# Optimization experiments

Measured on AMD Instinct MI355X. Metric: run time of the kernel, lower is better.

Reference implementation:

```python
import jax, jax.numpy as jnp
import numpy as np

EMBED_DIM = 512
NUM_HEADS = 8
B, L_Q, L_K = 2, 2048, 2048


def setup_inputs() -> dict:
    key = jax.random.key(0)
    ks = jax.random.split(key, 8)
    s = 0.02  # weight init scale
    return {
        "query": jax.random.normal(ks[0], (B, L_Q, EMBED_DIM), jnp.float32),
        "key":   jax.random.normal(ks[1], (B, L_K, EMBED_DIM), jnp.float32),
        "value": jax.random.normal(ks[2], (B, L_K, EMBED_DIM), jnp.float32),
        "wq": jax.random.normal(ks[3], (EMBED_DIM, EMBED_DIM), jnp.float32) * s,
        "wk": jax.random.normal(ks[4], (EMBED_DIM, EMBED_DIM), jnp.float32) * s,
        "wv": jax.random.normal(ks[5], (EMBED_DIM, EMBED_DIM), jnp.float32) * s,
        "bq": jnp.zeros((EMBED_DIM,), jnp.float32),
        "bk": jnp.zeros((EMBED_DIM,), jnp.float32),
        "bv": jnp.zeros((EMBED_DIM,), jnp.float32),
        "wo": jax.random.normal(ks[6], (EMBED_DIM, EMBED_DIM), jnp.float32) * s,
        "bo": jnp.zeros((EMBED_DIM,), jnp.float32),
    }


def _prob_sparse_mask(query, key, num_heads):
    # Faithful to _prob_QK: max-mean sparsity score, top-k query selection,
    # gather of reduced queries, reduced QK matmul (vectorized, no python loops).
    Bq, Lq, D = query.shape
    Lk = key.shape[1]
    dh = D // num_heads
    n_top = int(np.log(Lk))  # int(np.ceil/np.log) as in source forward: int(np.log(L_K))
    Q = query.reshape(Bq, Lq, num_heads, dh)
    K = key.reshape(Bq, Lk, num_heads, dh)
    Qh = jnp.transpose(Q, (0, 2, 1, 3))                      # [B,H,Lq,dh]
    # NOTE: source does K.transpose(1,2).reshape(B,H,D,L_K) -- a reshape, not a
    # transpose of the last two dims. We replicate that exactly.
    Kr = jnp.transpose(K, (0, 2, 1, 3)).reshape(Bq, num_heads, dh, Lk)  # [B,H,dh,Lk]
    QK = jnp.einsum('bhqd,bhdk->bhqk', Qh, Kr)               # [B,H,Lq,Lk]
    M = QK.max(-1) - QK.sum(-1) / Lk                         # max-mean score [B,H,Lq]
    _, M_top = jax.lax.top_k(M, n_top)                       # [B,H,n_top]
    Q_red = jnp.take_along_axis(Qh, M_top[..., None], axis=2)  # [B,H,n_top,dh]
    QK_red = jnp.einsum('bhtd,bhdk->bhtk', Q_red, Kr)        # [B,H,n_top,Lk]
    # Scatter reduced rows back into a full additive attn mask (zeros elsewhere).
    mask = jnp.zeros((Bq, num_heads, Lq, Lk), QK.dtype)
    bi = jnp.arange(Bq)[:, None, None]
    hi = jnp.arange(num_heads)[None, :, None]
    return mask.at[bi, hi, M_top].set(QK_red)


def reference(query, key, value, wq, wk, wv, bq, bk, bv, wo, bo):
    Bq, Lq, D = query.shape
    Lk = key.shape[1]
    H = NUM_HEADS
    dh = D // H
    mask = _prob_sparse_mask(query, key, H)                  # [B,H,Lq,Lk]
    q = (query @ wq.T + bq).reshape(Bq, Lq, H, dh).transpose(0, 2, 1, 3)
    k = (key @ wk.T + bk).reshape(Bq, Lk, H, dh).transpose(0, 2, 1, 3)
    v = (value @ wv.T + bv).reshape(Bq, Lk, H, dh).transpose(0, 2, 1, 3)
    scores = jnp.einsum('bhqd,bhkd->bhqk', q, k) * (dh ** -0.5) + mask
    attn = jax.nn.softmax(scores, axis=-1)                   # dropout inactive (eval)
    out = jnp.einsum('bhqk,bhkd->bhqd', attn, v)
    out = out.transpose(0, 2, 1, 3).reshape(Bq, Lq, D)
    return out @ wo.T + bo
```

## Files before the change

### kernel.cpp

```cpp
#include <hip/hip_runtime.h>
#include <type_traits>

#define DEV static __device__ __forceinline__

typedef short s16;
typedef __attribute__((ext_vector_type(4))) short short4_t;
typedef __attribute__((ext_vector_type(8))) short short8;
typedef __attribute__((ext_vector_type(4))) float f32x4;

#define NB 2
#define NH 8
#define SL 2048
#define DM 512
#define DH 64
#define NTOP 7
#define LOG2E 1.4426950408889634f
#define NROWS (NB*NH*SL)
#define FSPLIT 2
#define SSPLIT 2

DEV short f2bf(float x){
  union { float f; unsigned u; } v; v.f = x;
  unsigned r = v.u + 0x7fffu + ((v.u >> 16) & 1u);
  return (short)(r >> 16);
}
DEV float bf2f(short b){
  union { float f; unsigned u; } v; v.u = ((unsigned)(unsigned short)b) << 16;
  return v.f;
}
DEV f32x4 mfma16(short8 a, short8 b, f32x4 c){
  return __builtin_amdgcn_mfma_f32_16x16x32_bf16(a, b, c, 0, 0, 0);
}
DEV unsigned cvtpk(float lo, float hi){
  unsigned r;
  asm("v_cvt_pk_bf16_f32 %0, %1, %2" : "=v"(r) : "v"(lo), "v"(hi));
  return r;
}
DEV void gl2lds16(const s16* g, s16* l){
  __builtin_amdgcn_global_load_lds(
      (const __attribute__((address_space(1))) unsigned*)g,
      (__attribute__((address_space(3))) unsigned*)l, 16, 0, 0);
}

__global__ void prep_kernel(const float* __restrict__ query, const float* __restrict__ key,
    const float* __restrict__ value,
    const float* __restrict__ wq, const float* __restrict__ wk,
    const float* __restrict__ wv, const float* __restrict__ wo,
    s16* __restrict__ q_hi, s16* __restrict__ q_lo, s16* __restrict__ xk, s16* __restrict__ xv,
    s16* __restrict__ khi, s16* __restrict__ klo,
    s16* __restrict__ wqb, s16* __restrict__ wkb, s16* __restrict__ wvb, s16* __restrict__ wob){
  const int nbb = (NB*SL*DM)/256;
  const int wbb = (DM*DM)/256;
  __shared__ s16 thi[64][66];
  __shared__ s16 tlo[64][66];
  int bid = blockIdx.x;
  int t = threadIdx.x;
  if (bid < nbb){
    int i = bid*256 + t;
    float v = query[i];
    short h = f2bf(v);
    q_hi[i] = h;
    q_lo[i] = f2bf(v - bf2f(h));
    return;
  }
  bid -= nbb;
  if (bid < nbb){ int i = bid*256 + t; xk[i] = f2bf(key[i]); return; }
  bid -= nbb;
  if (bid < nbb){ int i = bid*256 + t; xv[i] = f2bf(value[i]); return; }
  bid -= nbb;
  if (bid < 512){
    int k6 = bid & 31, h = (bid >> 5) & 7, b = bid >> 8;
    int kl = t & 63, dq = t >> 6;
    #pragma unroll
    for (int dd = 0; dd < 16; ++dd){
      int d = dd*4 + dq;
      float v = key[((size_t)b*SL + d*32 + k6)*DM + h*DH + kl];
      short hh = f2bf(v);
      thi[d][kl] = hh;
      tlo[d][kl] = f2bf(v - bf2f(hh));
    }
    __syncthreads();
    int d2 = t & 63, kq = t >> 6;
    size_t obase = (((size_t)(b*NH + h))*SL + (size_t)k6*64)*DH;
    #pragma unroll
    for (int kk = 0; kk < 16; ++kk){
      int kl2 = kk*4 + kq;
      khi[obase + (size_t)kl2*DH + d2] = thi[d2][kl2];
      klo[obase + (size_t)kl2*DH + d2] = tlo[d2][kl2];
    }
    return;
  }
  bid -= 512;
  if (bid < wbb){ int i = bid*256 + t; wqb[i] = f2bf(wq[i]); return; }
  bid -= wbb;
  if (bid < wbb){ int i = bid*256 + t; wkb[i] = f2bf(wk[i]); return; }
  bid -= wbb;
  if (bid < wbb){ int i = bid*256 + t; wvb[i] = f2bf(wv[i]); return; }
  bid -= wbb;
  if (bid < wbb){ int i = bid*256 + t; wob[i] = f2bf(wo[i]); return; }
}

__global__ __launch_bounds__(256) void vpt_kernel(const s16* __restrict__ Vp, s16* __restrict__ VpT){
  __shared__ s16 tl[64][66];
  int bid = blockIdx.x;
  int k6 = bid & 31, h = (bid >> 5) & 7, b = bid >> 8;
  int t = threadIdx.x;
  int d = t & 63, kq = t >> 6;
  #pragma unroll
  for (int kk = 0; kk < 16; ++kk){
    int kl = kk*4 + kq;
    tl[kl][d] = Vp[((size_t)b*SL + k6*64 + kl)*DM + h*DH + d];
  }
  __syncthreads();
  int kl2 = t & 63, dq = t >> 6;
  size_t obase = ((size_t)(b*NH + h))*DH*SL + (size_t)k6*64;
  #pragma unroll
  for (int dd = 0; dd < 16; ++dd){
    int d2 = dd*4 + dq;
    VpT[obase + (size_t)d2*SL + kl2] = tl[kl2][d2];
  }
}

template<int OUTF32>
DEV void gemm_body(const s16* __restrict__ A, const s16* __restrict__ Bw,
        const float* __restrict__ bias, void* __restrict__ Cout, int bid, int tid, float scale){
  __shared__ __align__(16) s16 Abuf[2][128*64];
  __shared__ __align__(16) s16 Bbuf[2][64*64];
  int nt = bid >> 3, ot = bid & 7;
  int w = tid >> 6, l = tid & 63;
  int lr = l & 15, lg = l >> 4;
  int n0 = nt*128, o0 = ot*64;
  auto stage = [&](int cur, int kg){
    #pragma unroll
    for (int i = 0; i < 4; ++i){
      int r = w*32 + i*8 + (l>>3);
      int cs = (l&7) ^ (r&7);
      gl2lds16(A + (size_t)(n0 + r)*DM + kg + cs*8, &Abuf[cur][(w*32 + i*8)*64]);
    }
    #pragma unroll
    for (int i = 0; i < 2; ++i){
      int r = w*16 + i*8 + (l>>3);
      int cs = (l&7) ^ (r&7);
      gl2lds16(Bw + (size_t)(o0 + r)*DM + kg + cs*8, &Bbuf[cur][(w*16 + i*8)*64]);
    }
  };
  f32x4 acc[2][4] = {};
  stage(0, 0);
  __syncthreads();
  const int NIT = DM/64;
  for (int it = 0; it < NIT; ++it){
    int cur = it & 1;
    if (it + 1 < NIT) stage(cur^1, (it+1)*64);
    #pragma unroll
    for (int kc = 0; kc < 2; ++kc){
      short8 a0 = *(const short8*)&Abuf[cur][(w*32 +      lr)*64 + ((kc*4+lg) ^ (lr&7))*8];
      short8 a1 = *(const short8*)&Abuf[cur][(w*32 + 16 + lr)*64 + ((kc*4+lg) ^ (lr&7))*8];
      #pragma unroll
      for (int c = 0; c < 4; ++c){
        short8 bf = *(const short8*)&Bbuf[cur][(c*16 + lr)*64 + ((kc*4+lg) ^ (lr&7))*8];
        acc[0][c] = mfma16(a0, bf, acc[0][c]);
        acc[1][c] = mfma16(a1, bf, acc[1][c]);
      }
    }
    __syncthreads();
  }
  #pragma unroll
  for (int sub = 0; sub < 2; ++sub)
    #pragma unroll
    for (int c = 0; c < 4; ++c){
      int col = o0 + c*16 + lr;
      float bb = bias[col];
      #pragma unroll
      for (int j = 0; j < 4; ++j){
        int row = n0 + w*32 + sub*16 + lg*4 + j;
        float v = (acc[sub][c][j] + bb)*scale;
        if (OUTF32) ((float*)Cout)[(size_t)row*DM + col] = v;
        else        ((s16*) Cout)[(size_t)row*DM + col] = f2bf(v);
      }
    }
}

__global__ __launch_bounds__(256) void gemm_proj(const s16* __restrict__ Aq, const s16* __restrict__ Ak,
        const s16* __restrict__ Av, const s16* __restrict__ Wq, const s16* __restrict__ Wk,
        const s16* __restrict__ Wv, const float* __restrict__ bq, const float* __restrict__ bk,
        const float* __restrict__ bv, s16* __restrict__ Oq, s16* __restrict__ Ok, s16* __restrict__ Ov){
  int which = blockIdx.x >> 8;
  const s16* A  = which == 0 ? Aq : which == 1 ? Ak : Av;
  const s16* Bw = which == 0 ? Wq : which == 1 ? Wk : Wv;
  const float* bias = which == 0 ? bq : which == 1 ? bk : bv;
  s16* C = which == 0 ? Oq : which == 1 ? Ok : Ov;
  float scale = which == 0 ? 0.125f*LOG2E : 1.0f;
  gemm_body<0>(A, Bw, bias, C, blockIdx.x & 255, threadIdx.x, scale);
}

__global__ __launch_bounds__(256) void gemm_out(const s16* __restrict__ A, const s16* __restrict__ Bw,
        const float* __restrict__ bias, float* __restrict__ Cout){
  gemm_body<1>(A, Bw, bias, Cout, blockIdx.x, threadIdx.x, 1.0f);
}

__global__ __launch_bounds__(512) void stats_kernel(const s16* __restrict__ qhi, const s16* __restrict__ qlo,
        const s16* __restrict__ khi, const s16* __restrict__ klo,
        float* __restrict__ Mmx, float* __restrict__ Msm){
  __shared__ __align__(16) s16 Hbuf[2][64*64];
  __shared__ __align__(16) s16 Lbuf[2][64*64];
  int bid = blockIdx.x;
  int s = bid & 1, qt = (bid >> 1) & 15, h = (bid >> 5) & 7, b = bid >> 8;
  int tid = threadIdx.x;
  int w = tid >> 6, l = tid & 63;
  int lr = l & 15, lg = l >> 4;
  int dx = lr & 7;
  int q0 = qt*128 + w*16;
  const s16* qp  = qhi + ((size_t)b*SL + q0 + lr)*DM + h*DH + lg*8;
  const s16* qlp = qlo + ((size_t)b*SL + q0 + lr)*DM + h*DH + lg*8;
  short8 qh0 = *(const short8*)qp;
  short8 qh1 = *(const short8*)(qp + 32);
  short8 ql0 = *(const short8*)qlp;
  short8 ql1 = *(const short8*)(qlp + 32);
  const s16* kb  = khi + ((size_t)b*NH + h)*SL*DH;
  const s16* klb = klo + ((size_t)b*NH + h)*SL*DH;
  const s16* hR0 = &Hbuf[0][lr*64 + ((lg      ^ dx)*8)];
  const s16* hR1 = &Hbuf[0][lr*64 + (((4+lg) ^ dx)*8)];
  const s16* lR0 = &Lbuf[0][lr*64 + ((lg      ^ dx)*8)];
  const s16* lR1 = &Lbuf[0][lr*64 + (((4+lg) ^ dx)*8)];
  int rS = tid >> 3;
  int csK = (tid & 7) ^ (rS & 7);
  auto stage = [&](int cur, int kg){
    gl2lds16(kb  + (size_t)(kg + rS)*DH + csK*8, &Hbuf[cur][w*512]);
    gl2lds16(klb + (size_t)(kg + rS)*DH + csK*8, &Lbuf[cur][w*512]);
  };
  float mx = -1e30f, sm = 0.f;
  auto body = [&](auto CURC){
    constexpr int CUR = decltype(CURC)::value;
    #pragma unroll
    for (int t = 0; t < 4; ++t){
      short8 kh0 = *(const short8*)(hR0 + CUR*4096 + t*1024);
      short8 kh1 = *(const short8*)(hR1 + CUR*4096 + t*1024);
      short8 kl0 = *(const short8*)(lR0 + CUR*4096 + t*1024);
      short8 kl1 = *(const short8*)(lR1 + CUR*4096 + t*1024);
      f32x4 sacc = {};
      sacc = mfma16(kh0, qh0, sacc);
      sacc = mfma16(kh1, qh1, sacc);
      sacc = mfma16(kl0, qh0, sacc);
      sacc = mfma16(kl1, qh1, sacc);
      sacc = mfma16(kh0, ql0, sacc);
      sacc = mfma16(kh1, ql1, sacc);
      #pragma unroll
      for (int j = 0; j < 4; ++j){ mx = fmaxf(mx, sacc[j]); sm += sacc[j]; }
    }
  };
  int kbeg = s*(SL/SSPLIT);
  stage(0, kbeg);
  __syncthreads();
  #pragma unroll 1
  for (int i2 = 0; i2 < 8; ++i2){
    stage(1, kbeg + (2*i2+1)*64);
    body(std::integral_constant<int,0>{});
    __syncthreads();
    if (i2 < 7) stage(0, kbeg + (2*i2+2)*64);
    body(std::integral_constant<int,1>{});
    __syncthreads();
  }
  mx = fmaxf(mx, __shfl_xor(mx, 16));
  mx = fmaxf(mx, __shfl_xor(mx, 32));
  sm += __shfl_xor(sm, 16);
  sm += __shfl_xor(sm, 32);
  if (lg == 0){
    size_t row = ((size_t)b*NH + h)*SL + q0 + lr;
    Mmx[(size_t)s*NROWS + row] = mx;
    Msm[(size_t)s*NROWS + row] = sm;
  }
}

__global__ __launch_bounds__(256) void topk_kernel(const float* __restrict__ Mmx,
        const float* __restrict__ Msm, int* __restrict__ topidx, int* __restrict__ rowsel){
  int bh = blockIdx.x;
  int t = threadIdx.x;
  int w = t >> 6, l = t & 63;
  __shared__ float smv[SL];
  __shared__ float rv[4];
  __shared__ int   ri[4];
  size_t base = (size_t)bh*SL;
  for (int i = t; i < SL; i += 256){
    float mx = Mmx[base + i];
    float sm = Msm[base + i];
    #pragma unroll
    for (int s = 1; s < SSPLIT; ++s){
      mx = fmaxf(mx, Mmx[(size_t)s*NROWS + base + i]);
      sm += Msm[(size_t)s*NROWS + base + i];
    }
    smv[i] = mx - sm*(1.0f/SL);
    rowsel[base + i] = -1;
  }
  __syncthreads();
  for (int tt = 0; tt < NTOP; ++tt){
    float bvv = -1e38f; int bi = SL;
    for (int i = t; i < SL; i += 256){
      float v = smv[i];
      if (v > bvv){ bvv = v; bi = i; }
    }
    #pragma unroll
    for (int off = 32; off >= 1; off >>= 1){
      float ov = __shfl_xor(bvv, off);
      int oi = __shfl_xor(bi, off);
      if (ov > bvv || (ov == bvv && oi < bi)){ bvv = ov; bi = oi; }
    }
    if (l == 0){ rv[w] = bvv; ri[w] = bi; }
    __syncthreads();
    if (t == 0){
      float bv2 = rv[0]; int bi2 = ri[0];
      #pragma unroll
      for (int ww = 1; ww < 4; ++ww)
        if (rv[ww] > bv2 || (rv[ww] == bv2 && ri[ww] < bi2)){ bv2 = rv[ww]; bi2 = ri[ww]; }
      topidx[bh*8 + tt] = bi2;
      rowsel[base + bi2] = tt;
      smv[bi2] = -1e38f;
    }
    __syncthreads();
  }
}

__global__ __launch_bounds__(256) void maskrow_kernel(const float* __restrict__ query,
        const float* __restrict__ key, const int* __restrict__ topidx, float* __restrict__ maskrows){
  __shared__ float tile[64][65];
  __shared__ float qs[NTOP][64];
  int bid = blockIdx.x;
  int k6 = bid & 31, h = (bid >> 5) & 7, b = bid >> 8;
  int bh = b*NH + h;
  int t = threadIdx.x;
  int kl = t & 63, w = t >> 6;
  for (int i = t; i < NTOP*64; i += 256){
    int tt = i >> 6, d = i & 63;
    qs[tt][d] = query[((size_t)b*SL + topidx[bh*8 + tt])*DM + h*DH + d];
  }
  #pragma unroll
  for (int dd = 0; dd < 16; ++dd){
    int d = dd*4 + w;
    tile[d][kl] = key[((size_t)b*SL + d*32 + k6)*DM + h*DH + kl];
  }
  __syncthreads();
  for (int tt = w; tt < NTOP; tt += 4){
    float acc = 0.f;
    #pragma unroll
    for (int d = 0; d < 64; ++d)
      acc = fmaf(qs[tt][d], tile[d][kl], acc);
    maskrows[((size_t)bh*NTOP + tt)*SL + k6*64 + kl] = acc*LOG2E;
  }
}

__global__ __launch_bounds__(512) void flash_kernel(const s16* __restrict__ Qp, const s16* __restrict__ Kp,
        const s16* __restrict__ VpT, const float* __restrict__ maskrows, const int* __restrict__ rowsel,
        float* __restrict__ Opart, float* __restrict__ lpart){
  __shared__ __align__(16) s16 Kbuf[2][64*64];
  __shared__ __align__(16) s16 Vbuf[2][64*64];
  int bid = blockIdx.x;
  int s = bid & 1, qt = (bid >> 1) & 15, h = (bid >> 5) & 7, b = bid >> 8;
  int tid = threadIdx.x;
  int w = tid >> 6, l = tid & 63;
  int lr = l & 15, lg = l >> 4;
  int dx = lr & 7;
  int q0 = qt*128 + w*16;
  int bh = b*NH + h;
  const s16* qp = Qp + ((size_t)b*SL + q0 + lr)*DM + h*DH + lg*8;
  short8 bq0 = *(const short8*)qp;
  short8 bq1 = *(const short8*)(qp + 32);
  int sel = rowsel[(size_t)bh*SL + q0 + lr];
  const float* mrow = maskrows + ((size_t)bh*NTOP + (sel >= 0 ? sel : 0))*SL;
  const s16* kpb = Kp + (size_t)b*SL*DM + h*DH;
  const s16* vtb = VpT + (size_t)bh*DH*SL;
  const s16* kR0 = &Kbuf[0][lr*64 + ((lg      ^ dx)*8)];
  const s16* kR1 = &Kbuf[0][lr*64 + (((4+lg) ^ dx)*8)];
  const s16* vb0 = &Vbuf[0][lr*64];
  const int gL0 = ((0  + lg) ^ (dx<<1))*4;
  const int gH0 = ((4  + lg) ^ (dx<<1))*4;
  const int gL1 = ((8  + lg) ^ (dx<<1))*4;
  const int gH1 = ((12 + lg) ^ (dx<<1))*4;
  int rS = tid >> 3;
  int csK = (tid & 7) ^ (rS & 7);
  auto stage = [&](int cur, int kg){
    gl2lds16(kpb + (size_t)(kg + rS)*DM + csK*8, &Kbuf[cur][w*512]);
    gl2lds16(vtb + (size_t)rS*SL + kg + csK*8, &Vbuf[cur][w*512]);
  };
  f32x4 acc[4] = {};
  float lsum = 0.f;
  auto body = [&](auto CURC, int k0){
    constexpr int CUR = decltype(CURC)::value;
    float pv[4][4];
    #pragma unroll
    for (int t = 0; t < 4; ++t){
      short8 ka0 = *(const short8*)(kR0 + CUR*4096 + t*1024);
      short8 ka1 = *(const short8*)(kR1 + CUR*4096 + t*1024);
      f32x4 sc = {};
      sc = mfma16(ka0, bq0, sc);
      sc = mfma16(ka1, bq1, sc);
      #pragma unroll
      for (int j = 0; j < 4; ++j) pv[t][j] = sc[j];
    }
    if (sel >= 0){
      #pragma unroll
      for (int t = 0; t < 4; ++t)
        #pragma unroll
        for (int j = 0; j < 4; ++j)
          pv[t][j] += mrow[k0 + t*16 + lg*4 + j];
    }
    #pragma unroll
    for (int t = 0; t < 4; ++t)
      #pragma unroll
      for (int j = 0; j < 4; ++j){
        float pp = exp2f(pv[t][j]);
        pv[t][j] = pp;
        lsum += pp;
      }
    short8 paf[2];
    #pragma unroll
    for (int kt = 0; kt < 2; ++kt){
      union { unsigned u[4]; short8 s8; } uu;
      uu.u[0] = cvtpk(pv[2*kt][0],   pv[2*kt][1]);
      uu.u[1] = cvtpk(pv[2*kt][2],   pv[2*kt][3]);
      uu.u[2] = cvtpk(pv[2*kt+1][0], pv[2*kt+1][1]);
      uu.u[3] = cvtpk(pv[2*kt+1][2], pv[2*kt+1][3]);
      paf[kt] = uu.s8;
    }
    #pragma unroll
    for (int c = 0; c < 4; ++c){
      short4_t lo0 = *(const short4_t*)(vb0 + CUR*4096 + c*1024 + gL0);
      short4_t hi0 = *(const short4_t*)(vb0 + CUR*4096 + c*1024 + gH0);
      acc[c] = mfma16(__builtin_shufflevector(lo0, hi0, 0,1,2,3,4,5,6,7), paf[0], acc[c]);
      short4_t lo1 = *(const short4_t*)(vb0 + CUR*4096 + c*1024 + gL1);
      short4_t hi1 = *(const short4_t*)(vb0 + CUR*4096 + c*1024 + gH1);
      acc[c] = mfma16(__builtin_shufflevector(lo1, hi1, 0,1,2,3,4,5,6,7), paf[1], acc[c]);
    }
  };
  int kbeg = s*(SL/FSPLIT);
  stage(0, kbeg);
  __syncthreads();
  #pragma unroll 1
  for (int i2 = 0; i2 < 8; ++i2){
    stage(1, kbeg + (2*i2+1)*64);
    body(std::integral_constant<int,0>{}, kbeg + 2*i2*64);
    __syncthreads();
    if (i2 < 7) stage(0, kbeg + (2*i2+2)*64);
    body(std::integral_constant<int,1>{}, kbeg + (2*i2+1)*64);
    __syncthreads();
  }
  lsum += __shfl_xor(lsum, 16);
  lsum += __shfl_xor(lsum, 32);
  size_t row = (size_t)bh*SL + q0 + lr;
  float* Op = Opart + ((size_t)s*NROWS + row)*DH;
  #pragma unroll
  for (int c = 0; c < 4; ++c)
    *(f32x4*)(Op + c*16 + lg*4) = acc[c];
  if (lg == 0)
    lpart[(size_t)s*NROWS + row] = lsum;
}

__global__ __launch_bounds__(256) void flash_combine(const float* __restrict__ Opart,
        const float* __restrict__ lpart, s16* __restrict__ outh){
  int row = blockIdx.x*4 + (threadIdx.x >> 6);
  int d = threadIdx.x & 63;
  float L = lpart[row] + lpart[NROWS + row];
  float o = (Opart[(size_t)row*DH + d] + Opart[((size_t)NROWS + row)*DH + d]) / L;
  int b = row >> 14, h = (row >> 11) & 7, q = row & (SL - 1);
  outh[((size_t)b*SL + q)*DM + h*DH + d] = f2bf(o);
}

extern "C" void kernel_launch(void* const* d_in, const int* in_sizes, int n_in,
                              void* d_out, int out_size, void* d_ws, size_t ws_size,
                              hipStream_t stream){
  (void)in_sizes; (void)n_in; (void)out_size;
  const float* query = (const float*)d_in[0];
  const float* key   = (const float*)d_in[1];
  const float* value = (const float*)d_in[2];
  const float* wq    = (const float*)d_in[3];
  const float* wk    = (const float*)d_in[4];
  const float* wv    = (const float*)d_in[5];
  const float* bq    = (const float*)d_in[6];
  const float* bk    = (const float*)d_in[7];
  const float* bv    = (const float*)d_in[8];
  const float* wo    = (const float*)d_in[9];
  const float* bo    = (const float*)d_in[10];

  const size_t NE = (size_t)NB*SL*DM;
  const size_t WE = (size_t)DM*DM;

  char* p = (char*)d_ws;
  size_t off = 0;
  auto alloc = [&](size_t n)->char*{ char* r = p + off; off += (n + 255) & ~(size_t)255; return r; };
  s16* wob = (s16*)alloc(WE*2);
  s16* Qp  = (s16*)alloc(NE*2);
  s16* Kp  = (s16*)alloc(NE*2);
  s16* VpT = (s16*)alloc(NE*2);
  float* maskrows = (float*)alloc((size_t)NB*NH*NTOP*SL*4);
  int* topidx   = (int*)alloc((size_t)NB*NH*8*4);
  int* rowsel   = (int*)alloc((size_t)NROWS*4);
  float* Mmx    = (float*)alloc((size_t)SSPLIT*NROWS*4);
  float* Msm    = (float*)alloc((size_t)SSPLIT*NROWS*4);
  float* lpart  = (float*)alloc((size_t)FSPLIT*NROWS*4);
  s16* outh = (s16*)alloc(NE*2);
  size_t offA = off;
  s16* q_hi = (s16*)alloc(NE*2);
  s16* q_lo = (s16*)alloc(NE*2);
  s16* xk   = (s16*)alloc(NE*2);
  s16* xv   = (s16*)alloc(NE*2);
  s16* khatT_hi = (s16*)alloc(NE*2);
  s16* khatT_lo = (s16*)alloc(NE*2);
  s16* wqb = (s16*)alloc(WE*2);
  s16* wkb = (s16*)alloc(WE*2);
  s16* wvb = (s16*)alloc(WE*2);
  s16* Vp  = (s16*)alloc(NE*2);
  float* Opart = (float*)(p + offA);
  size_t needOpart = offA + (size_t)FSPLIT*NROWS*DH*4;
  if (off > ws_size || needOpart > ws_size) return;

  const int nbb = (int)(NE/256);
  const int wbb = (int)(WE/256);
  prep_kernel<<<3*nbb + 512 + 4*wbb, 256, 0, stream>>>(query, key, value, wq, wk, wv, wo,
      q_hi, q_lo, xk, xv, khatT_hi, khatT_lo, wqb, wkb, wvb, wob);

  gemm_proj<<<3*256, 256, 0, stream>>>(q_hi, xk, xv, wqb, wkb, wvb, bq, bk, bv, Qp, Kp, Vp);
  vpt_kernel<<<512, 256, 0, stream>>>(Vp, VpT);

  stats_kernel<<<NB*NH*(SL/128)*SSPLIT, 512, 0, stream>>>(q_hi, q_lo, khatT_hi, khatT_lo, Mmx, Msm);
  topk_kernel<<<NB*NH, 256, 0, stream>>>(Mmx, Msm, topidx, rowsel);
  maskrow_kernel<<<512, 256, 0, stream>>>(query, key, topidx, maskrows);

  flash_kernel<<<NB*NH*(SL/128)*FSPLIT, 512, 0, stream>>>(Qp, Kp, VpT, maskrows, rowsel,
      Opart, lpart);
  flash_combine<<<NROWS/4, 256, 0, stream>>>(Opart, lpart, outh);
  gemm_out<<<256, 256, 0, stream>>>(outh, wob, bo, (float*)d_out);
}
```

Measured before the change: 139.9 us.

## Quadruple key-split in stats and flash kernels; permute V^T for vector LDS reads

Raises the key-dimension split for both the sparsity-stats and flash attention kernels from 2 to 4. This doubles the grid so more blocks can run concurrently, at the cost of more partial outputs and a heavier combine step. The V transpose kernel now writes keys in a permuted order so the flash kernel can load each V fragment with one 16-byte swizzled LDS read instead of two 8-byte reads and a shuffle. It also splits the row-sum into four independent accumulators and gives Opart its own workspace slot instead of aliasing freed buffers, which increases workspace use.

Result: no change. 141.3 us (+1.0%).

```diff
diff --git a/kernel.cpp b/kernel.cpp
--- a/kernel.cpp
+++ b/kernel.cpp
@@ -16,8 +16,8 @@
 #define NTOP 7
 #define LOG2E 1.4426950408889634f
 #define NROWS (NB*NH*SL)
-#define FSPLIT 2
-#define SSPLIT 2
+#define FSPLIT 4
+#define SSPLIT 4
 
 DEV short f2bf(float x){
   union { float f; unsigned u; } v; v.f = x;
@@ -113,11 +113,12 @@
   }
   __syncthreads();
   int kl2 = t & 63, dq = t >> 6;
+  int kp = (kl2 & 32) + ((kl2 >> 2) & 3)*8 + (kl2 & 3) + ((kl2 >> 4) & 1)*4;
   size_t obase = ((size_t)(b*NH + h))*DH*SL + (size_t)k6*64;
   #pragma unroll
   for (int dd = 0; dd < 16; ++dd){
     int d2 = dd*4 + dq;
-    VpT[obase + (size_t)d2*SL + kl2] = tl[kl2][d2];
+    VpT[obase + (size_t)d2*SL + kp] = tl[kl2][d2];
   }
 }
 
@@ -204,7 +205,7 @@
   __shared__ __align__(16) s16 Hbuf[2][64*64];
   __shared__ __align__(16) s16 Lbuf[2][64*64];
   int bid = blockIdx.x;
-  int s = bid & 1, qt = (bid >> 1) & 15, h = (bid >> 5) & 7, b = bid >> 8;
+  int s = bid & 3, qt = (bid >> 2) & 15, h = (bid >> 6) & 7, b = bid >> 9;
   int tid = threadIdx.x;
   int w = tid >> 6, l = tid & 63;
   int lr = l & 15, lg = l >> 4;
@@ -249,14 +250,15 @@
     }
   };
   int kbeg = s*(SL/SSPLIT);
+  const int NI2 = (SL/SSPLIT)/128;
   stage(0, kbeg);
   __syncthreads();
   #pragma unroll 1
-  for (int i2 = 0; i2 < 8; ++i2){
+  for (int i2 = 0; i2 < NI2; ++i2){
     stage(1, kbeg + (2*i2+1)*64);
     body(std::integral_constant<int,0>{});
     __syncthreads();
-    if (i2 < 7) stage(0, kbeg + (2*i2+2)*64);
+    if (i2 < NI2-1) stage(0, kbeg + (2*i2+2)*64);
     body(std::integral_constant<int,1>{});
     __syncthreads();
   }
@@ -353,7 +355,7 @@
   __shared__ __align__(16) s16 Kbuf[2][64*64];
   __shared__ __align__(16) s16 Vbuf[2][64*64];
   int bid = blockIdx.x;
-  int s = bid & 1, qt = (bid >> 1) & 15, h = (bid >> 5) & 7, b = bid >> 8;
+  int s = bid & 3, qt = (bid >> 2) & 15, h = (bid >> 6) & 7, b = bid >> 9;
   int tid = threadIdx.x;
   int w = tid >> 6, l = tid & 63;
   int lr = l & 15, lg = l >> 4;
@@ -369,11 +371,8 @@
   const s16* vtb = VpT + (size_t)bh*DH*SL;
   const s16* kR0 = &Kbuf[0][lr*64 + ((lg      ^ dx)*8)];
   const s16* kR1 = &Kbuf[0][lr*64 + (((4+lg) ^ dx)*8)];
-  const s16* vb0 = &Vbuf[0][lr*64];
-  const int gL0 = ((0  + lg) ^ (dx<<1))*4;
-  const int gH0 = ((4  + lg) ^ (dx<<1))*4;
-  const int gL1 = ((8  + lg) ^ (dx<<1))*4;
-  const int gH1 = ((12 + lg) ^ (dx<<1))*4;
+  const s16* vR0 = &Vbuf[0][lr*64 + ((lg      ^ dx)*8)];
+  const s16* vR1 = &Vbuf[0][lr*64 + (((4+lg) ^ dx)*8)];
   int rS = tid >> 3;
   int csK = (tid & 7) ^ (rS & 7);
   auto stage = [&](int cur, int kg){
@@ -381,7 +380,7 @@
     gl2lds16(vtb + (size_t)rS*SL + kg + csK*8, &Vbuf[cur][w*512]);
   };
   f32x4 acc[4] = {};
-  float lsum = 0.f;
+  float ls0 = 0.f, ls1 = 0.f, ls2 = 0.f, ls3 = 0.f;
   auto body = [&](auto CURC, int k0){
     constexpr int CUR = decltype(CURC)::value;
     float pv[4][4];
@@ -403,13 +402,12 @@
           pv[t][j] += mrow[k0 + t*16 + lg*4 + j];
     }
     #pragma unroll
-    for (int t = 0; t < 4; ++t)
-      #pragma unroll
-      for (int j = 0; j < 4; ++j){
-        float pp = exp2f(pv[t][j]);
-        pv[t][j] = pp;
-        lsum += pp;
-      }
+    for (int t = 0; t < 4; ++t){
+      pv[t][0] = exp2f(pv[t][0]); ls0 += pv[t][0];
+      pv[t][1] = exp2f(pv[t][1]); ls1 += pv[t][1];
+      pv[t][2] = exp2f(pv[t][2]); ls2 += pv[t][2];
+      pv[t][3] = exp2f(pv[t][3]); ls3 += pv[t][3];
+    }
     short8 paf[2];
     #pragma unroll
     for (int kt = 0; kt < 2; ++kt){
@@ -422,26 +420,26 @@
     }
     #pragma unroll
     for (int c = 0; c < 4; ++c){
-      short4_t lo0 = *(const short4_t*)(vb0 + CUR*4096 + c*1024 + gL0);
-      short4_t hi0 = *(const short4_t*)(vb0 + CUR*4096 + c*1024 + gH0);
-      acc[c] = mfma16(__builtin_shufflevector(lo0, hi0, 0,1,2,3,4,5,6,7), paf[0], acc[c]);
-      short4_t lo1 = *(const short4_t*)(vb0 + CUR*4096 + c*1024 + gL1);
-      short4_t hi1 = *(const short4_t*)(vb0 + CUR*4096 + c*1024 + gH1);
-      acc[c] = mfma16(__builtin_shufflevector(lo1, hi1, 0,1,2,3,4,5,6,7), paf[1], acc[c]);
+      short8 vf0 = *(const short8*)(vR0 + CUR*4096 + c*1024);
+      acc[c] = mfma16(vf0, paf[0], acc[c]);
+      short8 vf1 = *(const short8*)(vR1 + CUR*4096 + c*1024);
+      acc[c] = mfma16(vf1, paf[1], acc[c]);
     }
   };
   int kbeg = s*(SL/FSPLIT);
+  const int NI2 = (SL/FSPLIT)/128;
   stage(0, kbeg);
   __syncthreads();
   #pragma unroll 1
-  for (int i2 = 0; i2 < 8; ++i2){
+  for (int i2 = 0; i2 < NI2; ++i2){
     stage(1, kbeg + (2*i2+1)*64);
     body(std::integral_constant<int,0>{}, kbeg + 2*i2*64);
     __syncthreads();
-    if (i2 < 7) stage(0, kbeg + (2*i2+2)*64);
+    if (i2 < NI2-1) stage(0, kbeg + (2*i2+2)*64);
     body(std::integral_constant<int,1>{}, kbeg + (2*i2+1)*64);
     __syncthreads();
   }
+  float lsum = (ls0 + ls1) + (ls2 + ls3);
   lsum += __shfl_xor(lsum, 16);
   lsum += __shfl_xor(lsum, 32);
   size_t row = (size_t)bh*SL + q0 + lr;
@@ -457,8 +455,13 @@
         const float* __restrict__ lpart, s16* __restrict__ outh){
   int row = blockIdx.x*4 + (threadIdx.x >> 6);
   int d = threadIdx.x & 63;
-  float L = lpart[row] + lpart[NROWS + row];
-  float o = (Opart[(size_t)row*DH + d] + Opart[((size_t)NROWS + row)*DH + d]) / L;
+  float L = 0.f, o = 0.f;
+  #pragma unroll
+  for (int s = 0; s < FSPLIT; ++s){
+    L += lpart[(size_t)s*NROWS + row];
+    o += Opart[((size_t)s*NROWS + row)*DH + d];
+  }
+  o /= L;
   int b = row >> 14, h = (row >> 11) & 7, q = row & (SL - 1);
   outh[((size_t)b*SL + q)*DM + h*DH + d] = f2bf(o);
 }
@@ -495,8 +498,8 @@
   float* Mmx    = (float*)alloc((size_t)SSPLIT*NROWS*4);
   float* Msm    = (float*)alloc((size_t)SSPLIT*NROWS*4);
   float* lpart  = (float*)alloc((size_t)FSPLIT*NROWS*4);
+  float* Opart  = (float*)alloc((size_t)FSPLIT*NROWS*DH*4);
   s16* outh = (s16*)alloc(NE*2);
-  size_t offA = off;
   s16* q_hi = (s16*)alloc(NE*2);
   s16* q_lo = (s16*)alloc(NE*2);
   s16* xk   = (s16*)alloc(NE*2);
@@ -507,9 +510,7 @@
   s16* wkb = (s16*)alloc(WE*2);
   s16* wvb = (s16*)alloc(WE*2);
   s16* Vp  = (s16*)alloc(NE*2);
-  float* Opart = (float*)(p + offA);
-  size_t needOpart = offA + (size_t)FSPLIT*NROWS*DH*4;
-  if (off > ws_size || needOpart > ws_size) return;
+  if (off > ws_size) return;
 
   const int nbb = (int)(NE/256);
   const int wbb = (int)(WE/256);
```
